# Kernel optimization log

Hardware: AMD Instinct MI355X
Metric: run time of the kernel (lower is better)

The kernel has to match this reference:

```python
import jax, jax.numpy as jnp
import numpy as np

B, S, D = 8, 1024, 768
H = 12
HD = D // H  # 64
SCALE = 1.0 / (HD ** 0.5)


def setup_inputs() -> dict:
    key = jax.random.key(0)
    ks = jax.random.split(key, 5)
    x = jax.random.normal(ks[0], (B, S, D), dtype=jnp.float32)
    W_qkv = jax.random.normal(ks[1], (D, 3 * D), dtype=jnp.float32) * 0.02
    b_qkv = jax.random.normal(ks[2], (3 * D,), dtype=jnp.float32) * 0.02
    W_proj = jax.random.normal(ks[3], (D, D), dtype=jnp.float32) * 0.02
    b_proj = jax.random.normal(ks[4], (D,), dtype=jnp.float32) * 0.02
    return {"x": x, "W_qkv": W_qkv, "b_qkv": b_qkv, "W_proj": W_proj, "b_proj": b_proj}


def reference(x, W_qkv, b_qkv, W_proj, b_proj):
    b, s, d = x.shape
    # QKV projection: (B, S, 3D) -> (3, B, H, S, HD)
    qkv = x @ W_qkv + b_qkv
    qkv = qkv.reshape(b, s, 3, H, HD).transpose(2, 0, 3, 1, 4)
    q, k, v = qkv[0], qkv[1], qkv[2]
    # scaled dot-product attention (full matrix, as in the original)
    scores = jnp.einsum("bhqd,bhkd->bhqk", q, k) * SCALE
    attn = jax.nn.softmax(scores, axis=-1)
    out = jnp.einsum("bhqk,bhkd->bhqd", attn, v)
    # merge heads: (B, S, D)
    out = out.transpose(0, 2, 1, 3).reshape(b, s, d)
    return out @ W_proj + b_proj
```

## Files before the change

kernel.cpp:

```cpp
#include <hip/hip_runtime.h>
#include <math.h>

typedef __attribute__((ext_vector_type(8))) unsigned short ushortx8;
typedef __attribute__((ext_vector_type(8))) __bf16 bf16x8;
typedef __attribute__((ext_vector_type(4))) float floatx4;
typedef __attribute__((ext_vector_type(16))) float floatx16;

#define NH 12
#define SEQ 1024
#define DM 768
#define HD 64
#define GK 768
#define QK_SCALE 0.18033688011112042f

#define GLDS16(gp, lp) __builtin_amdgcn_global_load_lds( \
    (const __attribute__((address_space(1))) unsigned int*)(const void*)(gp), \
    (__attribute__((address_space(3))) unsigned int*)(lp), 16, 0, 0)

__device__ __forceinline__ unsigned short f2bf(float f) {
    union { float f; unsigned u; } v; v.f = f;
    unsigned r = v.u + 0x7fffu + ((v.u >> 16) & 1u);
    return (unsigned short)(r >> 16);
}

__device__ __forceinline__ unsigned pk2bf(float f0, float f1) {
    union { float f; unsigned u; } a, b; a.f = f0; b.f = f1;
    return ((a.u + 0x8000u) >> 16) | ((b.u + 0x8000u) & 0xffff0000u);
}

__global__ void k_prep(const float* __restrict__ x, unsigned short* __restrict__ x_bf,
                       const float* __restrict__ Wqkv, unsigned short* __restrict__ WqkvT,
                       const float* __restrict__ Wproj, unsigned short* __restrict__ WprojT) {
    __shared__ float tile[32][33];
    int bx = blockIdx.x;
    if (bx < 6144) {
        int i = bx * 256 + threadIdx.x;
        float4 v = ((const float4*)x)[i];
        ushort4 o;
        o.x = f2bf(v.x); o.y = f2bf(v.y); o.z = f2bf(v.z); o.w = f2bf(v.w);
        ((ushort4*)x_bf)[i] = o;
        return;
    }
    const float* in; unsigned short* out; int R, C, c0, r0;
    if (bx < 7872) {
        int t = bx - 6144;
        in = Wqkv; out = WqkvT; R = 768; C = 2304;
        c0 = (t % 72) * 32; r0 = (t / 72) * 32;
    } else {
        int t = bx - 7872;
        in = Wproj; out = WprojT; R = 768; C = 768;
        c0 = (t % 24) * 32; r0 = (t / 24) * 32;
    }
    int tx = threadIdx.x & 31, ty = threadIdx.x >> 5;
#pragma unroll
    for (int i = 0; i < 4; i++)
        tile[ty + 8 * i][tx] = in[(size_t)(r0 + ty + 8 * i) * C + c0 + tx];
    __syncthreads();
#pragma unroll
    for (int i = 0; i < 4; i++)
        out[(size_t)(c0 + ty + 8 * i) * R + r0 + tx] = f2bf(tile[tx][ty + 8 * i]);
}


__device__ __forceinline__ void stage6(const unsigned short* gA, const unsigned short* gB,
                                       unsigned short* lbuf, int w, int k0) {
#pragma unroll
    for (int g = 0; g < 4; g++)
        GLDS16(gA + (size_t)(w * 64 + g * 16) * GK + k0, lbuf + (w * 64 + g * 16) * 32);
#pragma unroll
    for (int g = 0; g < 2; g++)
        GLDS16(gB + (size_t)(w * 32 + g * 16) * GK + k0, lbuf + 8192 + (w * 32 + g * 16) * 32);
}

__device__ __forceinline__ void mfma24(const unsigned short* Ab, const unsigned short* Bb,
                                       int wm, int wn, int l15, int csw,
                                       floatx4 (&acc)[8][3]) {
    bf16x8 af[8], bfr[3];
#pragma unroll
    for (int m = 0; m < 8; m++)
        af[m] = __builtin_bit_cast(bf16x8,
            *(const ushortx8*)&Ab[(wm * 128 + m * 16 + l15) * 32 + csw]);
#pragma unroll
    for (int n = 0; n < 3; n++)
        bfr[n] = __builtin_bit_cast(bf16x8,
            *(const ushortx8*)&Bb[(wn * 48 + n * 16 + l15) * 32 + csw]);
#pragma unroll
    for (int m = 0; m < 8; m++)
#pragma unroll
        for (int n = 0; n < 3; n++)
            acc[m][n] = __builtin_amdgcn_mfma_f32_16x16x32_bf16(af[m], bfr[n], acc[m][n], 0, 0, 0);
}

__device__ __forceinline__ void gemm_mainloop(const unsigned short* __restrict__ A,
                                              const unsigned short* __restrict__ Bt,
                                              unsigned short* smem, int m0, int n0,
                                              int w, int lane, floatx4 (&acc)[8][3]) {
    int quad = lane >> 4, l15 = lane & 15;
    int wm = w >> 1, wn = w & 1;
    int rA = lane >> 2;
    int cSwz = ((lane & 3) ^ ((lane >> 3) & 3)) * 8;
    int csw = (quad ^ ((l15 >> 1) & 3)) * 8;
    const unsigned short* gA = A + (size_t)(m0 + rA) * GK + cSwz;
    const unsigned short* gB = Bt + (size_t)(n0 + rA) * GK + cSwz;

    stage6(gA, gB, smem, w, 0);
    stage6(gA, gB, smem + 12288, w, 32);
#pragma unroll 1
    for (int t = 0; t < 24; t++) {
        if (t < 23) asm volatile("s_waitcnt vmcnt(6)" ::: "memory");
        else        asm volatile("s_waitcnt vmcnt(0)" ::: "memory");
        __builtin_amdgcn_s_barrier();
        asm volatile("" ::: "memory");
        const unsigned short* Ab = smem + (t & 1) * 12288;
        __builtin_amdgcn_s_setprio(1);
        mfma24(Ab, Ab + 8192, wm, wn, l15, csw, acc);
        __builtin_amdgcn_s_setprio(0);
        asm volatile("" ::: "memory");
        __builtin_amdgcn_s_barrier();
        asm volatile("" ::: "memory");
        if (t < 22) stage6(gA, gB, smem + (t & 1) * 12288, w, (t + 2) * 32);
    }
}

__global__ __launch_bounds__(256, 3) void k_gemm_qkv(
    const unsigned short* __restrict__ A, const unsigned short* __restrict__ Bt,
    const float* __restrict__ bias,
    unsigned short* __restrict__ Qb, unsigned short* __restrict__ Kb,
    unsigned short* __restrict__ Vt) {
    __shared__ unsigned short smem[25344];
    int tid = threadIdx.x;
    int w = tid >> 6, lane = tid & 63;
    int quad = lane >> 4, l15 = lane & 15;
    int wm = w >> 1, wn = w & 1;
    int lin = blockIdx.x;
    int xcd = lin & 7, slot = lin >> 3;
    int mt_i = xcd * 4 + (slot & 3);
    int nt_i = slot >> 2;
    int m0 = mt_i * 256, n0 = nt_i * 96;

    floatx4 acc[8][3] = {};
    gemm_mainloop(A, Bt, smem, m0, n0, w, lane, acc);

    int tsel = nt_i / 8;
    int bb = m0 >> 10;
    int s_base0 = (m0 & 1023) + wm * 128;
    if (tsel < 2) {
        unsigned short* __restrict__ dst = (tsel == 0) ? Qb : Kb;
#pragma unroll
        for (int m = 0; m < 8; m++) {
            int s_base = s_base0 + m * 16 + quad * 4;
#pragma unroll
            for (int n = 0; n < 3; n++) {
                int n_g = n0 + wn * 48 + n * 16 + l15;
                int nloc = n_g - tsel * 768;
                int hh = nloc >> 6, dd = nloc & 63;
                float bv = bias[n_g];
                size_t base = ((size_t)(bb * NH + hh) * SEQ + s_base) * HD + dd;
                if (tsel == 0) {
#pragma unroll
                    for (int rg = 0; rg < 4; rg++)
                        dst[base + (size_t)rg * HD] = f2bf((acc[m][n][rg] + bv) * QK_SCALE);
                } else {
#pragma unroll
                    for (int rg = 0; rg < 4; rg++)
                        dst[base + (size_t)rg * HD] = f2bf(acc[m][n][rg] + bv);
                }
            }
        }
    } else {
        __syncthreads();
#pragma unroll
        for (int m = 0; m < 8; m++) {
#pragma unroll
            for (int n = 0; n < 3; n++) {
                int col = wn * 48 + n * 16 + l15;
                float bv = bias[n0 + col];
                ushort4 pk;
                pk.x = f2bf(acc[m][n][0] + bv);
                pk.y = f2bf(acc[m][n][1] + bv);
                pk.z = f2bf(acc[m][n][2] + bv);
                pk.w = f2bf(acc[m][n][3] + bv);
                *(ushort4*)&smem[col * 264 + wm * 128 + m * 16 + quad * 4] = pk;
            }
        }
        __syncthreads();
        if (tid < 192) {
            int col = tid >> 1, part = tid & 1;
            int dglob = (n0 - 1536) + col;
            int hh = dglob >> 6, dd = dglob & 63;
            size_t gbase = ((size_t)(bb * NH + hh) * HD + dd) * SEQ + (m0 & 1023) + part * 128;
#pragma unroll
            for (int i = 0; i < 16; i++)
                *(uint4*)&Vt[gbase + i * 8] = *(const uint4*)&smem[col * 264 + part * 128 + i * 8];
        }
    }
}

__global__ __launch_bounds__(256) void k_attn(
    const unsigned short* __restrict__ Qb, const unsigned short* __restrict__ Kb,
    const unsigned short* __restrict__ Vt, unsigned short* __restrict__ attn_out) {
    __shared__ unsigned short Ks[64 * 64];
    __shared__ unsigned short Vts[64 * 64];
    __shared__ unsigned short Pt[4][32 * 72];
    int tid = threadIdx.x;
    int w = tid >> 6, lane = tid & 63;
    int l31 = lane & 31, lh = lane >> 5;
    int lin = blockIdx.x;
    int xcd = lin & 7, slot = lin >> 3;
    int bh = xcd * 12 + (slot >> 3);
    int qt = slot & 7;
    int b = bh / NH, h = bh - b * NH;
    const unsigned short* Qp = Qb + (size_t)bh * SEQ * HD;
    const unsigned short* Kp = Kb + (size_t)bh * SEQ * HD;
    const unsigned short* Vp = Vt + (size_t)bh * HD * SEQ;
    int q0w = qt * 128 + w * 32;
    unsigned short* Ptw = &Pt[w][0];

    bf16x8 qf[4];
#pragma unroll
    for (int ds = 0; ds < 4; ds++)
        qf[ds] = __builtin_bit_cast(bf16x8,
            *(const ushortx8*)&Qp[(size_t)(q0w + l31) * HD + ds * 16 + lh * 8]);

    floatx16 o[2] = {};
    float lsum = 0.f;

    int rr = tid >> 3, cc8 = (tid & 7) * 8;
    int cs = cc8 ^ ((rr & 7) * 8);
    int rsw = (l31 & 7) * 8;
    uint4 kr0 = *(const uint4*)&Kp[(size_t)rr * HD + cc8];
    uint4 kr1 = *(const uint4*)&Kp[(size_t)(rr + 32) * HD + cc8];
    uint4 vr0 = *(const uint4*)&Vp[(size_t)rr * SEQ + cc8];
    uint4 vr1 = *(const uint4*)&Vp[(size_t)(rr + 32) * SEQ + cc8];

    for (int kb = 0; kb < SEQ; kb += 64) {
        __syncthreads();
        *(uint4*)&Ks[rr * 64 + cs] = kr0;
        *(uint4*)&Ks[(rr + 32) * 64 + cs] = kr1;
        *(uint4*)&Vts[rr * 64 + cs] = vr0;
        *(uint4*)&Vts[(rr + 32) * 64 + cs] = vr1;
        if (kb + 64 < SEQ) {
            kr0 = *(const uint4*)&Kp[(size_t)(kb + 64 + rr) * HD + cc8];
            kr1 = *(const uint4*)&Kp[(size_t)(kb + 64 + rr + 32) * HD + cc8];
            vr0 = *(const uint4*)&Vp[(size_t)rr * SEQ + kb + 64 + cc8];
            vr1 = *(const uint4*)&Vp[(size_t)(rr + 32) * SEQ + kb + 64 + cc8];
        }
        __syncthreads();

        floatx16 sc[2] = {};
        __builtin_amdgcn_s_setprio(1);
#pragma unroll
        for (int mt = 0; mt < 2; mt++)
#pragma unroll
            for (int ds = 0; ds < 4; ds++) {
                bf16x8 kf = __builtin_bit_cast(bf16x8,
                    *(const ushortx8*)&Ks[(mt * 32 + l31) * 64 + ((ds * 16 + lh * 8) ^ rsw)]);
                sc[mt] = __builtin_amdgcn_mfma_f32_32x32x16_bf16(kf, qf[ds], sc[mt], 0, 0, 0);
            }
        __builtin_amdgcn_s_setprio(0);

        float p0[16], p1[16];
#pragma unroll
        for (int r = 0; r < 16; r++) {
            p0[r] = exp2f(sc[0][r]);
            p1[r] = exp2f(sc[1][r]);
            lsum += p0[r] + p1[r];
        }

        uint4 pw[4];
#pragma unroll
        for (int mt = 0; mt < 2; mt++) {
            const float* pp = mt ? p1 : p0;
#pragma unroll
            for (int hf = 0; hf < 2; hf++) {
                unsigned a, bq, c, d;
                asm("v_cvt_pk_bf16_f32 %0, %1, %2" : "=v"(a)  : "v"(pp[hf * 8 + 0]), "v"(pp[hf * 8 + 1]));
                asm("v_cvt_pk_bf16_f32 %0, %1, %2" : "=v"(bq) : "v"(pp[hf * 8 + 4]), "v"(pp[hf * 8 + 5]));
                asm("v_cvt_pk_bf16_f32 %0, %1, %2" : "=v"(c)  : "v"(pp[hf * 8 + 2]), "v"(pp[hf * 8 + 3]));
                asm("v_cvt_pk_bf16_f32 %0, %1, %2" : "=v"(d)  : "v"(pp[hf * 8 + 6]), "v"(pp[hf * 8 + 7]));
                asm("v_permlane32_swap_b32 %0, %1" : "+v"(a), "+v"(bq));
                asm("v_permlane32_swap_b32 %0, %1" : "+v"(c), "+v"(d));
                uint4 wv; wv.x = a; wv.y = c; wv.z = bq; wv.w = d;
                pw[mt * 2 + hf] = wv;
            }
        }

        __builtin_amdgcn_s_setprio(1);
#pragma unroll
        for (int ks = 0; ks < 4; ks++) {
            bf16x8 pf = __builtin_bit_cast(bf16x8, pw[ks]);
#pragma unroll
            for (int mt = 0; mt < 2; mt++) {
                bf16x8 vf = __builtin_bit_cast(bf16x8,
                    *(const ushortx8*)&Vts[(mt * 32 + l31) * 64 + ((ks * 16 + lh * 8) ^ rsw)]);
                o[mt] = __builtin_amdgcn_mfma_f32_32x32x16_bf16(vf, pf, o[mt], 0, 0, 0);
            }
        }
        __builtin_amdgcn_s_setprio(0);
    }

    lsum += __shfl_xor(lsum, 32, 64);
    float inv = 1.0f / lsum;

#pragma unroll
    for (int mt = 0; mt < 2; mt++)
#pragma unroll
        for (int g = 0; g < 4; g++) {
            uint2 pk;
            pk.x = pk2bf(o[mt][g * 4 + 0] * inv, o[mt][g * 4 + 1] * inv);
            pk.y = pk2bf(o[mt][g * 4 + 2] * inv, o[mt][g * 4 + 3] * inv);
            *(uint2*)&Ptw[l31 * 72 + mt * 32 + g * 8 + lh * 4] = pk;
        }
    __builtin_amdgcn_s_barrier();
#pragma unroll
    for (int pass = 0; pass < 4; pass++) {
        int row = pass * 8 + (lane >> 3);
        int col8 = (lane & 7) * 8;
        uint4 vv = *(const uint4*)&Ptw[row * 72 + col8];
        *(uint4*)&attn_out[(size_t)(b * SEQ + q0w + row) * DM + h * HD + col8] = vv;
    }
}

__global__ __launch_bounds__(256, 3) void k_gemm_proj(
    const unsigned short* __restrict__ A, const unsigned short* __restrict__ Bt,
    const float* __restrict__ bias, float* __restrict__ out) {
    __shared__ unsigned short smem[24576];
    int tid = threadIdx.x;
    int w = tid >> 6, lane = tid & 63;
    int quad = lane >> 4, l15 = lane & 15;
    int wm = w >> 1, wn = w & 1;
    int lin = blockIdx.x;
    int xcd = lin & 7, slot = lin >> 3;
    int mt_i = xcd * 4 + (slot & 3);
    int nt_i = slot >> 2;
    int m0 = mt_i * 256, n0 = nt_i * 96;

    floatx4 acc[8][3] = {};
    gemm_mainloop(A, Bt, smem, m0, n0, w, lane, acc);

#pragma unroll
    for (int m = 0; m < 8; m++) {
        int m_base = m0 + wm * 128 + m * 16 + quad * 4;
#pragma unroll
        for (int n = 0; n < 3; n++) {
            int n_g = n0 + wn * 48 + n * 16 + l15;
            float bv = bias[n_g];
#pragma unroll
            for (int rg = 0; rg < 4; rg++)
                out[(size_t)(m_base + rg) * DM + n_g] = acc[m][n][rg] + bv;
        }
    }
}

extern "C" void kernel_launch(void* const* d_in, const int* in_sizes, int n_in,
                              void* d_out, int out_size, void* d_ws, size_t ws_size,
                              hipStream_t stream) {
    const float* x     = (const float*)d_in[0];
    const float* Wqkv  = (const float*)d_in[1];
    const float* bqkv  = (const float*)d_in[2];
    const float* Wproj = (const float*)d_in[3];
    const float* bproj = (const float*)d_in[4];
    float* out = (float*)d_out;

    char* ws = (char*)d_ws;
    unsigned short* x_bf   = (unsigned short*)(ws);
    unsigned short* WqkvT  = (unsigned short*)(ws + 12582912);
    unsigned short* WprojT = (unsigned short*)(ws + 16121856);
    unsigned short* Qb     = (unsigned short*)(ws + 17301504);
    unsigned short* Kb     = (unsigned short*)(ws + 29884416);
    unsigned short* Vt     = (unsigned short*)(ws + 42467328);
    unsigned short* attn   = (unsigned short*)(ws + 55050240);

    k_prep<<<8448, 256, 0, stream>>>(x, x_bf, Wqkv, WqkvT, Wproj, WprojT);
    k_gemm_qkv<<<768, 256, 0, stream>>>(x_bf, WqkvT, bqkv, Qb, Kb, Vt);
    k_attn<<<768, 256, 0, stream>>>(Qb, Kb, Vt, attn);
    k_gemm_proj<<<256, 256, 0, stream>>>(attn, WprojT, bproj, out);
}
```

Before: 192.9 us.

## Load K and V MFMA fragments directly from global memory, dropping LDS staging

The attention kernel no longer stages K and V tiles through shared memory with two block-wide barriers per iteration. Each wave now loads its own K and V MFMA operand fragments straight from global memory into registers, prefetching the next K tile while V is loaded for the current step. This removes the LDS writes, the reads and the __syncthreads. In exchange each of the four waves fetches the same K/V data separately, which quadruples global/L2 traffic, raises register pressure, and exposes the V load latency inside the loop.

```diff
diff --git a/kernel.cpp b/kernel.cpp
--- a/kernel.cpp
+++ b/kernel.cpp
@@ -199,8 +199,6 @@
 __global__ __launch_bounds__(256) void k_attn(
     const unsigned short* __restrict__ Qb, const unsigned short* __restrict__ Kb,
     const unsigned short* __restrict__ Vt, unsigned short* __restrict__ attn_out) {
-    __shared__ unsigned short Ks[64 * 64];
-    __shared__ unsigned short Vts[64 * 64];
     __shared__ unsigned short Pt[4][32 * 72];
     int tid = threadIdx.x;
     int w = tid >> 6, lane = tid & 63;
@@ -222,42 +220,38 @@
         qf[ds] = __builtin_bit_cast(bf16x8,
             *(const ushortx8*)&Qp[(size_t)(q0w + l31) * HD + ds * 16 + lh * 8]);
 
+    const unsigned short* kbase = Kp + (size_t)l31 * HD + lh * 8;
+    const unsigned short* vbase = Vp + (size_t)l31 * SEQ + lh * 8;
+
     floatx16 o[2] = {};
     float lsum = 0.f;
 
-    int rr = tid >> 3, cc8 = (tid & 7) * 8;
-    int cs = cc8 ^ ((rr & 7) * 8);
-    int rsw = (l31 & 7) * 8;
-    uint4 kr0 = *(const uint4*)&Kp[(size_t)rr * HD + cc8];
-    uint4 kr1 = *(const uint4*)&Kp[(size_t)(rr + 32) * HD + cc8];
-    uint4 vr0 = *(const uint4*)&Vp[(size_t)rr * SEQ + cc8];
-    uint4 vr1 = *(const uint4*)&Vp[(size_t)(rr + 32) * SEQ + cc8];
-
+    uint4 kf[8];
+#pragma unroll
+    for (int i = 0; i < 8; i++)
+        kf[i] = *(const uint4*)&kbase[(size_t)((i >> 2) * 32) * HD + (i & 3) * 16];
+
+#pragma unroll 1
     for (int kb = 0; kb < SEQ; kb += 64) {
-        __syncthreads();
-        *(uint4*)&Ks[rr * 64 + cs] = kr0;
-        *(uint4*)&Ks[(rr + 32) * 64 + cs] = kr1;
-        *(uint4*)&Vts[rr * 64 + cs] = vr0;
-        *(uint4*)&Vts[(rr + 32) * 64 + cs] = vr1;
-        if (kb + 64 < SEQ) {
-            kr0 = *(const uint4*)&Kp[(size_t)(kb + 64 + rr) * HD + cc8];
-            kr1 = *(const uint4*)&Kp[(size_t)(kb + 64 + rr + 32) * HD + cc8];
-            vr0 = *(const uint4*)&Vp[(size_t)rr * SEQ + kb + 64 + cc8];
-            vr1 = *(const uint4*)&Vp[(size_t)(rr + 32) * SEQ + kb + 64 + cc8];
-        }
-        __syncthreads();
-
         floatx16 sc[2] = {};
         __builtin_amdgcn_s_setprio(1);
 #pragma unroll
         for (int mt = 0; mt < 2; mt++)
 #pragma unroll
-            for (int ds = 0; ds < 4; ds++) {
-                bf16x8 kf = __builtin_bit_cast(bf16x8,
-                    *(const ushortx8*)&Ks[(mt * 32 + l31) * 64 + ((ds * 16 + lh * 8) ^ rsw)]);
-                sc[mt] = __builtin_amdgcn_mfma_f32_32x32x16_bf16(kf, qf[ds], sc[mt], 0, 0, 0);
-            }
+            for (int ds = 0; ds < 4; ds++)
+                sc[mt] = __builtin_amdgcn_mfma_f32_32x32x16_bf16(
+                    __builtin_bit_cast(bf16x8, kf[mt * 4 + ds]), qf[ds], sc[mt], 0, 0, 0);
         __builtin_amdgcn_s_setprio(0);
+
+        if (kb + 64 < SEQ) {
+#pragma unroll
+            for (int i = 0; i < 8; i++)
+                kf[i] = *(const uint4*)&kbase[(size_t)(kb + 64 + (i >> 2) * 32) * HD + (i & 3) * 16];
+        }
+        uint4 vf[8];
+#pragma unroll
+        for (int i = 0; i < 8; i++)
+            vf[i] = *(const uint4*)&vbase[(size_t)((i & 1) * 32) * SEQ + kb + (i >> 1) * 16];
 
         float p0[16], p1[16];
 #pragma unroll
@@ -290,11 +284,9 @@
         for (int ks = 0; ks < 4; ks++) {
             bf16x8 pf = __builtin_bit_cast(bf16x8, pw[ks]);
 #pragma unroll
-            for (int mt = 0; mt < 2; mt++) {
-                bf16x8 vf = __builtin_bit_cast(bf16x8,
-                    *(const ushortx8*)&Vts[(mt * 32 + l31) * 64 + ((ks * 16 + lh * 8) ^ rsw)]);
-                o[mt] = __builtin_amdgcn_mfma_f32_32x32x16_bf16(vf, pf, o[mt], 0, 0, 0);
-            }
+            for (int mt = 0; mt < 2; mt++)
+                o[mt] = __builtin_amdgcn_mfma_f32_32x32x16_bf16(
+                    __builtin_bit_cast(bf16x8, vf[ks * 2 + mt]), pf, o[mt], 0, 0, 0);
         }
         __builtin_amdgcn_s_setprio(0);
     }
```

Result: slower. 234.0 us (+21.3%).
